# Performance work log

Measured on AMD Instinct MI355X. Metric: run time of the kernel, lower is better.

The kernel has to match this reference:

```python
import jax, jax.numpy as jnp
import numpy as np

N_NODES = 20000
N_EDGES = 160000
IN_DIM = 2048
HID = 512


def setup_inputs() -> dict:
    key = jax.random.key(0)
    ks = jax.random.split(key, 12)
    s1 = 1.0 / np.sqrt(IN_DIM)
    s2 = 1.0 / np.sqrt(HID)
    return {
        "x": jax.random.normal(ks[0], (N_NODES, IN_DIM), dtype=jnp.float32),
        "edge_index": jax.random.randint(ks[1], (2, N_EDGES), 0, N_NODES, dtype=jnp.int64),
        "W1": jax.random.uniform(ks[2], (IN_DIM, HID), jnp.float32, -s1, s1),
        "b1": jax.random.uniform(ks[3], (HID,), jnp.float32, -s1, s1),
        "W2": jax.random.uniform(ks[4], (HID, HID), jnp.float32, -s2, s2),
        "b2": jax.random.uniform(ks[5], (HID,), jnp.float32, -s2, s2),
        "Wg": jax.random.uniform(ks[6], (HID, HID), jnp.float32, -s2, s2),
        "bg": jax.random.uniform(ks[7], (HID,), jnp.float32, -s2, s2),
        "Wa": jax.random.uniform(ks[8], (HID, 1), jnp.float32, -s2, s2),
        "ba": jax.random.uniform(ks[9], (1,), jnp.float32, -s2, s2),
    }


def reference(x, edge_index, W1, b1, W2, b2, Wg, bg, Wa, ba):
    # GINConv (eps=0): h = MLP((1+eps)*x + sum_{j in N(i)} x_j)
    src, dst = edge_index[0], edge_index[1]
    agg = jax.ops.segment_sum(x[src], dst, num_segments=x.shape[0])  # [N, IN_DIM]
    h = x + agg
    h = jnp.maximum(h @ W1 + b1, 0.0) @ W2 + b2  # [N, HID]
    # Gated attention pooling scores
    A = jnp.tanh(h @ Wg + bg)                    # [N, HID]
    alpha = (A @ Wa + ba)[:, 0]                  # [N]
    att_scores = jax.nn.softmax(alpha, axis=0)   # softmax over all nodes
    return (h, att_scores)
```

## Files before the change

kernel.cpp:

```cpp
#include <hip/hip_runtime.h>

typedef __attribute__((ext_vector_type(8))) __bf16 bf16x8;
typedef __attribute__((ext_vector_type(4))) __bf16 bf16x4;
typedef __attribute__((ext_vector_type(4))) float f32x4;
typedef __attribute__((ext_vector_type(8))) unsigned short u16x8;

__device__ __forceinline__ bf16x8 cvt8(float4 a, float4 b) {
    bf16x8 o;
    o[0] = (__bf16)a.x; o[1] = (__bf16)a.y; o[2] = (__bf16)a.z; o[3] = (__bf16)a.w;
    o[4] = (__bf16)b.x; o[5] = (__bf16)b.y; o[6] = (__bf16)b.z; o[7] = (__bf16)b.w;
    return o;
}
__device__ __forceinline__ bf16x4 cvt4(f32x4 v) {
    bf16x4 o;
    o[0] = (__bf16)v[0]; o[1] = (__bf16)v[1]; o[2] = (__bf16)v[2]; o[3] = (__bf16)v[3];
    return o;
}

__device__ __forceinline__ unsigned swz(int row, int s) {
    return (unsigned)((row * 64 + s * 16) ^ ((row & 8) << 2));
}

__global__ __launch_bounds__(256) void convw_pre_kernel(const float* __restrict__ W,
                                                        char* __restrict__ out, int K) {
    int t = blockIdx.x * 256 + threadIdx.x;
    if (t >= K * 512) return;
    int k = t >> 9, n = t & 511;
    int cb = n >> 8, r = n & 255, tt = k >> 5, s = (k & 31) >> 3, e = k & 7;
    size_t off = ((size_t)cb * (K >> 5) + tt) * 16384 + swz(r, s) + e * 2;
    *(__bf16*)(out + off) = (__bf16)W[t];
}

__global__ __launch_bounds__(256) void count_kernel(const int* __restrict__ dst,
                                                    int* __restrict__ counts, int E) {
    int e = blockIdx.x * 256 + threadIdx.x;
    if (e < E) atomicAdd(&counts[dst[e]], 1);
}

__global__ __launch_bounds__(1024) void scan_kernel(const int* __restrict__ counts,
                                                    int* __restrict__ offs, int N) {
    __shared__ int wsum[16], wpre[16];
    const int CH = 20;
    int tid = threadIdx.x, lane = tid & 63, wv = tid >> 6;
    int base = tid * CH;
    int s = 0;
    for (int i = 0; i < CH; i++) { int idx = base + i; s += (idx < N) ? counts[idx] : 0; }
    int run = s;
#pragma unroll
    for (int o = 1; o < 64; o <<= 1) { int v = __shfl_up(run, o, 64); if (lane >= o) run += v; }
    if (lane == 63) wsum[wv] = run;
    __syncthreads();
    if (tid == 0) { int acc = 0; for (int w = 0; w < 16; w++) { wpre[w] = acc; acc += wsum[w]; } }
    __syncthreads();
    int pre = wpre[wv] + (run - s);
    for (int i = 0; i < CH; i++) {
        int idx = base + i;
        if (idx <= N) offs[idx] = pre;
        pre += (idx < N) ? counts[idx] : 0;
    }
}

__global__ __launch_bounds__(256) void bucket_kernel(const int* __restrict__ src,
                                                     const int* __restrict__ dst,
                                                     const int* __restrict__ offs,
                                                     int* __restrict__ cursor,
                                                     int* __restrict__ eids, int E) {
    int e = blockIdx.x * 256 + threadIdx.x;
    if (e >= E) return;
    int d = dst[e];
    int pos = atomicAdd(&cursor[d], 1);
    eids[offs[d] + pos] = src[e];
}

__global__ __launch_bounds__(256) void addy_kernel(const __bf16* __restrict__ y0,
                                                   const __bf16* __restrict__ y1,
                                                   __bf16* __restrict__ y) {
    size_t i = ((size_t)blockIdx.x * 256 + threadIdx.x) * 8;
    bf16x8 a = *(const bf16x8*)(y0 + i);
    bf16x8 b = *(const bf16x8*)(y1 + i);
    bf16x8 o;
#pragma unroll
    for (int j = 0; j < 8; j++) o[j] = (__bf16)((float)a[j] + (float)b[j]);
    *(bf16x8*)(y + i) = o;
}

__global__ __launch_bounds__(256) void gather_h1_kernel(const __bf16* __restrict__ y,
                                                        const int* __restrict__ offs,
                                                        const int* __restrict__ eids,
                                                        const float* __restrict__ b1,
                                                        __bf16* __restrict__ h1b) {
    const int node = blockIdx.x * 4 + (threadIdx.x >> 6);
    const int c = (threadIdx.x & 63) * 8;
    float s[8];
    bf16x8 v = *(const bf16x8*)(y + (size_t)node * 512 + c);
#pragma unroll
    for (int j = 0; j < 8; j++) s[j] = (float)v[j];
    const int beg = offs[node], end = offs[node + 1];
    for (int k = beg; k < end; k++) {
        int sn = eids[k];
        bf16x8 u = *(const bf16x8*)(y + (size_t)sn * 512 + c);
#pragma unroll
        for (int j = 0; j < 8; j++) s[j] += (float)u[j];
    }
    bf16x8 o;
#pragma unroll
    for (int j = 0; j < 8; j++) o[j] = (__bf16)fmaxf(s[j] + b1[c + j], 0.f);
    *(bf16x8*)(h1b + (size_t)node * 512 + c) = o;
}

__global__ __launch_bounds__(256) void gemm1_kernel(const float* __restrict__ X,
                                                    const char* __restrict__ Bpre,
                                                    __bf16* __restrict__ Ybase, int M) {
    constexpr int KDIM = 2048, NT2 = 16;
    __shared__ char smem[16384];
    const int tid = threadIdx.x, lane = tid & 63, wv = tid >> 6;
    const int fr = lane & 15, sec = lane >> 4, hi4 = (lane >> 4) * 4;
    const long row0 = (long)blockIdx.x * 64;
    const int kh = blockIdx.z;
    const char* Bp = Bpre + ((size_t)blockIdx.y * 64 + (size_t)kh * 32) * 16384;
    __bf16* Y = Ybase + (size_t)kh * 10240000;

    f32x4 acc[4][4];
#pragma unroll
    for (int m = 0; m < 4; m++)
#pragma unroll
        for (int n = 0; n < 4; n++)
#pragma unroll
            for (int r = 0; r < 4; r++) acc[m][n][r] = 0.f;

    const int ar_ = tid >> 2, ks = tid & 3;
    const unsigned awz = swz(ar_, ks);
    long arow = row0 + ar_; if (arow > (long)M - 1) arow = M - 1;
    const float* Ap = X + arow * KDIM + kh * 1024;

#define ASEC(b) (smem + (b) * 8192)
#define LOAD_A4(d0, d1, d2, d3, t) do {                      \
        const float* p_ = Ap + (t) * 64 + ks * 8;            \
        d0 = *(const float4*)(p_);                           \
        d1 = *(const float4*)(p_ + 4);                       \
        d2 = *(const float4*)(p_ + 32);                      \
        d3 = *(const float4*)(p_ + 36);                      \
    } while (0)

    {
        float4 a0, a1, a2, a3;
        LOAD_A4(a0, a1, a2, a3, 0);
        *(bf16x8*)(ASEC(0) + awz) = cvt8(a0, a1);
        *(bf16x8*)(ASEC(0) + 4096 + awz) = cvt8(a2, a3);
    }
    asm volatile("s_waitcnt lgkmcnt(0)" ::: "memory");
    __builtin_amdgcn_s_barrier();

    int cur = 0;
    for (int tt = 0; tt < NT2; tt++) {
        const bool more = (tt + 1 < NT2);
        float4 a0, a1, a2, a3;
        if (more) LOAD_A4(a0, a1, a2, a3, tt + 1);
#pragma unroll
        for (int h = 0; h < 2; h++) {
            const char* bt = Bp + (size_t)(tt * 2 + h) * 16384;
            bf16x8 wf[4], xf[4];
#pragma unroll
            for (int m = 0; m < 4; m++)
                wf[m] = *(const bf16x8*)(bt + swz(wv * 64 + m * 16 + fr, sec));
#pragma unroll
            for (int n = 0; n < 4; n++)
                xf[n] = *(const bf16x8*)(ASEC(cur) + h * 4096 + swz(n * 16 + fr, sec));
#pragma unroll
            for (int m = 0; m < 4; m++)
#pragma unroll
                for (int n = 0; n < 4; n++)
                    acc[m][n] = __builtin_amdgcn_mfma_f32_16x16x32_bf16(wf[m], xf[n], acc[m][n], 0, 0, 0);
        }
        if (more) {
            const int nxt = cur ^ 1;
            *(bf16x8*)(ASEC(nxt) + awz) = cvt8(a0, a1);
            *(bf16x8*)(ASEC(nxt) + 4096 + awz) = cvt8(a2, a3);
            asm volatile("s_waitcnt lgkmcnt(0)" ::: "memory");
            __builtin_amdgcn_s_barrier();
            cur = nxt;
        }
    }
#undef ASEC
#undef LOAD_A4

#pragma unroll
    for (int n = 0; n < 4; n++) {
        long node = row0 + n * 16 + fr;
        if (node < M) {
#pragma unroll
            for (int m = 0; m < 4; m++) {
                int col = blockIdx.y * 256 + wv * 64 + m * 16 + hi4;
                *(bf16x4*)(Y + node * 512 + col) = cvt4(acc[m][n]);
            }
        }
    }
}

__global__ __launch_bounds__(512) void mlp23_kernel(const __bf16* __restrict__ H1,
                                                    const char* __restrict__ W2p,
                                                    const float* __restrict__ b2,
                                                    const char* __restrict__ Wgp,
                                                    const float* __restrict__ bg,
                                                    const float* __restrict__ Wa,
                                                    float* __restrict__ Hout,
                                                    float* __restrict__ alpha) {
    constexpr int NT2 = 8;
    __shared__ char smem[41216];
    char* Hs = smem + 8192;
    float* aS = (float*)(smem + 40960);
    const int tid = threadIdx.x, lane = tid & 63, wv = tid >> 6;
    const int fr = lane & 15, sec = lane >> 4, hi4 = (lane >> 4) * 4;
    const long row0 = (long)blockIdx.x * 32;
    const int cbv = wv >> 2, rbase = (wv & 3) * 64;

    if (tid < 32) aS[tid] = 0.f;

    const int b16 = tid * 16;
    const int sh = b16 >> 11;
    const int bb = b16 & 2047;
    const int srow = bb >> 6;
    const int soff = bb & 63;
    const int ss = (soff ^ ((srow & 8) << 2)) >> 4;
    const __bf16* ApH = H1 + (row0 + srow) * 512 + sh * 32 + ss * 8;

#define ASEC(b) (smem + (b) * 4096)

    f32x4 acc[4][2];
#pragma unroll
    for (int m = 0; m < 4; m++)
#pragma unroll
        for (int n = 0; n < 2; n++)
#pragma unroll
            for (int r = 0; r < 4; r++) acc[m][n][r] = 0.f;

    if (tid < 256) {
        u16x8 v = *(const u16x8*)(ApH);
        *(u16x8*)(ASEC(0) + b16) = v;
    }
    asm volatile("s_waitcnt lgkmcnt(0)" ::: "memory");
    __builtin_amdgcn_s_barrier();

    int cur = 0;
    for (int tt = 0; tt < NT2; tt++) {
        u16x8 av;
        const bool more = (tt + 1 < NT2);
        if (more && tid < 256) av = *(const u16x8*)(ApH + (tt + 1) * 64);
#pragma unroll
        for (int h = 0; h < 2; h++) {
            const char* bt = W2p + ((size_t)cbv * 16 + tt * 2 + h) * 16384;
            bf16x8 wf[4], xf[2];
#pragma unroll
            for (int m = 0; m < 4; m++)
                wf[m] = *(const bf16x8*)(bt + swz(rbase + m * 16 + fr, sec));
#pragma unroll
            for (int n = 0; n < 2; n++)
                xf[n] = *(const bf16x8*)(ASEC(cur) + h * 2048 + swz(n * 16 + fr, sec));
#pragma unroll
            for (int m = 0; m < 4; m++)
#pragma unroll
                for (int n = 0; n < 2; n++)
                    acc[m][n] = __builtin_amdgcn_mfma_f32_16x16x32_bf16(wf[m], xf[n], acc[m][n], 0, 0, 0);
        }
        if (more) {
            const int nxt = cur ^ 1;
            if (tid < 256) *(u16x8*)(ASEC(nxt) + b16) = av;
            asm volatile("s_waitcnt lgkmcnt(0)" ::: "memory");
            __builtin_amdgcn_s_barrier();
            cur = nxt;
        }
    }

#pragma unroll
    for (int n = 0; n < 2; n++) {
        int node = n * 16 + fr;
        long gnode = row0 + node;
#pragma unroll
        for (int m = 0; m < 4; m++) {
            int hc = wv * 64 + m * 16 + hi4;
            f32x4 bv = *(const f32x4*)(b2 + hc);
            f32x4 v = acc[m][n] + bv;
            *(f32x4*)(Hout + gnode * 512 + hc) = v;
            int tt = hc >> 5, sk = (hc & 31) >> 3, e = hc & 7;
            *(bf16x4*)(Hs + tt * 2048 + swz(node, sk) + e * 2) = cvt4(v);
        }
    }
    asm volatile("s_waitcnt lgkmcnt(0)" ::: "memory");
    __builtin_amdgcn_s_barrier();

    f32x4 acc2[4][2];
#pragma unroll
    for (int m = 0; m < 4; m++)
#pragma unroll
        for (int n = 0; n < 2; n++)
#pragma unroll
            for (int r = 0; r < 4; r++) acc2[m][n][r] = 0.f;

    for (int g = 0; g < 16; g++) {
        const char* bt = Wgp + ((size_t)cbv * 16 + g) * 16384;
        bf16x8 wf[4], xf[2];
#pragma unroll
        for (int m = 0; m < 4; m++)
            wf[m] = *(const bf16x8*)(bt + swz(rbase + m * 16 + fr, sec));
#pragma unroll
        for (int n = 0; n < 2; n++)
            xf[n] = *(const bf16x8*)(Hs + g * 2048 + swz(n * 16 + fr, sec));
#pragma unroll
        for (int m = 0; m < 4; m++)
#pragma unroll
            for (int n = 0; n < 2; n++)
                acc2[m][n] = __builtin_amdgcn_mfma_f32_16x16x32_bf16(wf[m], xf[n], acc2[m][n], 0, 0, 0);
    }
#undef ASEC

#pragma unroll
    for (int n = 0; n < 2; n++) {
        float s = 0.f;
#pragma unroll
        for (int m = 0; m < 4; m++) {
            int gc = wv * 64 + m * 16 + hi4;
            f32x4 bgv = *(const f32x4*)(bg + gc);
            f32x4 wav = *(const f32x4*)(Wa + gc);
#pragma unroll
            for (int r = 0; r < 4; r++)
                s += tanhf(acc2[m][n][r] + bgv[r]) * wav[r];
        }
        s += __shfl_xor(s, 16, 64);
        s += __shfl_xor(s, 32, 64);
        if (sec == 0) atomicAdd(&aS[n * 16 + fr], s);
    }
    __syncthreads();
    if (tid < 32) alpha[row0 + tid] = aS[tid];
}

__global__ __launch_bounds__(1024) void softmax_kernel(const float* __restrict__ alpha,
                                                       float* __restrict__ att, int N) {
    __shared__ float red[16];
    __shared__ float bc[2];
    int tid = threadIdx.x, lane = tid & 63, wv = tid >> 6;
    float m = -3.4e38f;
    for (int i = tid; i < N; i += 1024) m = fmaxf(m, alpha[i]);
#pragma unroll
    for (int o = 32; o > 0; o >>= 1) m = fmaxf(m, __shfl_xor(m, o, 64));
    if (lane == 0) red[wv] = m;
    __syncthreads();
    if (tid == 0) {
        float mm = red[0];
        for (int i = 1; i < 16; i++) mm = fmaxf(mm, red[i]);
        bc[0] = mm;
    }
    __syncthreads();
    float Mx = bc[0];
    float s = 0.f;
    for (int i = tid; i < N; i += 1024) s += expf(alpha[i] - Mx);
#pragma unroll
    for (int o = 32; o > 0; o >>= 1) s += __shfl_xor(s, o, 64);
    if (lane == 0) red[wv] = s;
    __syncthreads();
    if (tid == 0) {
        float ss = 0.f;
        for (int i = 0; i < 16; i++) ss += red[i];
        bc[1] = ss;
    }
    __syncthreads();
    float inv = 1.f / bc[1];
    for (int i = tid; i < N; i += 1024) att[i] = expf(alpha[i] - Mx) * inv;
}

extern "C" void kernel_launch(void* const* d_in, const int* in_sizes, int n_in,
                              void* d_out, int out_size, void* d_ws, size_t ws_size,
                              hipStream_t stream) {
    const float* x  = (const float*)d_in[0];
    const int*   ei = (const int*)d_in[1];
    const float* W1 = (const float*)d_in[2];
    const float* b1 = (const float*)d_in[3];
    const float* W2 = (const float*)d_in[4];
    const float* b2 = (const float*)d_in[5];
    const float* Wg = (const float*)d_in[6];
    const float* bg = (const float*)d_in[7];
    const float* Wa = (const float*)d_in[8];

    const int M = 20000, IN = 2048, H = 512, E = 160000;

    char* ws = (char*)d_ws;
    __bf16* yp    = (__bf16*)ws;
    __bf16* ysum  = (__bf16*)(ws + 40960000);
    char*  W1p    = ws + 61440000;
    char*  W2p    = ws + 63537152;
    char*  Wgp    = ws + 64061440;
    __bf16* h1b   = (__bf16*)(ws + 64585728);
    float* alpha  = (float*)(ws + 85065728);
    int*   counts = (int*)(ws + 85145728);
    int*   offs   = (int*)(ws + 85225728);
    int*   cursor = (int*)(ws + 85305732);
    int*   eids   = (int*)(ws + 85385732);

    float* hout = (float*)d_out;
    float* att  = hout + (size_t)M * H;

    convw_pre_kernel<<<4096, 256, 0, stream>>>(W1, W1p, IN);
    convw_pre_kernel<<<1024, 256, 0, stream>>>(W2, W2p, H);
    convw_pre_kernel<<<1024, 256, 0, stream>>>(Wg, Wgp, H);

    hipMemsetAsync(counts, 0, M * 4, stream);
    count_kernel<<<(E + 255) / 256, 256, 0, stream>>>(ei + E, counts, E);
    scan_kernel<<<1, 1024, 0, stream>>>(counts, offs, M);
    hipMemsetAsync(cursor, 0, M * 4, stream);
    bucket_kernel<<<(E + 255) / 256, 256, 0, stream>>>(ei, ei + E, offs, cursor, eids, E);

    gemm1_kernel<<<dim3(313, 2, 2), 256, 0, stream>>>(x, W1p, yp, M);
    addy_kernel<<<5000, 256, 0, stream>>>(yp, yp + 10240000, ysum);

    gather_h1_kernel<<<5000, 256, 0, stream>>>(ysum, offs, eids, b1, h1b);

    mlp23_kernel<<<625, 512, 0, stream>>>(h1b, W2p, b2, Wgp, bg, Wa, hout, alpha);

    softmax_kernel<<<1, 1024, 0, stream>>>(alpha, att, M);
}
```

Baseline: 290.1 us.

## Restructure gemm1 to 4-way split-K with full A tile staged in LDS

The first GEMM now uses 512-thread blocks that load the whole 64x512 A slice, converted to bf16, into 64KB of LDS up front. The K dimension is split into four chunks instead of two, and the double-buffered A pipeline is replaced by a single barrier. Each block now covers all 512 output columns across 8 waves, so every A load is shared by both column halves and x is read from global memory only once. The cost is four bf16 partial outputs, which doubles the partial-sum traffic summed by addy4, plus a larger LDS footprint that may reduce occupancy. The global loads no longer overlap with the MFMA work.

```diff
diff --git a/kernel.cpp b/kernel.cpp
--- a/kernel.cpp
+++ b/kernel.cpp
@@ -72,15 +72,17 @@
     eids[offs[d] + pos] = src[e];
 }
 
-__global__ __launch_bounds__(256) void addy_kernel(const __bf16* __restrict__ y0,
-                                                   const __bf16* __restrict__ y1,
-                                                   __bf16* __restrict__ y) {
+__global__ __launch_bounds__(256) void addy4_kernel(const __bf16* __restrict__ p,
+                                                    __bf16* __restrict__ y) {
     size_t i = ((size_t)blockIdx.x * 256 + threadIdx.x) * 8;
-    bf16x8 a = *(const bf16x8*)(y0 + i);
-    bf16x8 b = *(const bf16x8*)(y1 + i);
+    bf16x8 a = *(const bf16x8*)(p + i);
+    bf16x8 b = *(const bf16x8*)(p + 10240000 + i);
+    bf16x8 c = *(const bf16x8*)(p + 20480000 + i);
+    bf16x8 d = *(const bf16x8*)(p + 30720000 + i);
     bf16x8 o;
 #pragma unroll
-    for (int j = 0; j < 8; j++) o[j] = (__bf16)((float)a[j] + (float)b[j]);
+    for (int j = 0; j < 8; j++)
+        o[j] = (__bf16)(((float)a[j] + (float)b[j]) + ((float)c[j] + (float)d[j]));
     *(bf16x8*)(y + i) = o;
 }
 
@@ -108,18 +110,32 @@
     *(bf16x8*)(h1b + (size_t)node * 512 + c) = o;
 }
 
-__global__ __launch_bounds__(256) void gemm1_kernel(const float* __restrict__ X,
-                                                    const char* __restrict__ Bpre,
-                                                    __bf16* __restrict__ Ybase, int M) {
-    constexpr int KDIM = 2048, NT2 = 16;
-    __shared__ char smem[16384];
+__global__ __launch_bounds__(512, 4) void gemm1_kernel(const float* __restrict__ X,
+                                                       const char* __restrict__ Bpre,
+                                                       __bf16* __restrict__ Ybase, int M) {
+    extern __shared__ char smem[];
     const int tid = threadIdx.x, lane = tid & 63, wv = tid >> 6;
     const int fr = lane & 15, sec = lane >> 4, hi4 = (lane >> 4) * 4;
     const long row0 = (long)blockIdx.x * 64;
-    const int kh = blockIdx.z;
-    const char* Bp = Bpre + ((size_t)blockIdx.y * 64 + (size_t)kh * 32) * 16384;
+    const int kh = blockIdx.y;
+    const int cb = wv >> 2, rbase = (wv & 3) * 64;
+    const char* Bp = Bpre + ((size_t)cb * 64 + (size_t)kh * 16) * 16384;
     __bf16* Y = Ybase + (size_t)kh * 10240000;
 
+#pragma unroll
+    for (int j = 0; j < 8; j++) {
+        int b = tid * 16 + j * 8192;
+        int tt = b >> 12, bb = b & 4095;
+        int row = bb >> 6, soff = bb & 63;
+        int s = (soff ^ ((row & 8) << 2)) >> 4;
+        long arow = row0 + row; if (arow > (long)M - 1) arow = M - 1;
+        const float* p = X + arow * 2048 + kh * 512 + tt * 32 + s * 8;
+        float4 a0 = *(const float4*)p;
+        float4 a1 = *(const float4*)(p + 4);
+        *(bf16x8*)(smem + b) = cvt8(a0, a1);
+    }
+    __syncthreads();
+
     f32x4 acc[4][4];
 #pragma unroll
     for (int m = 0; m < 4; m++)
@@ -128,61 +144,22 @@
 #pragma unroll
             for (int r = 0; r < 4; r++) acc[m][n][r] = 0.f;
 
-    const int ar_ = tid >> 2, ks = tid & 3;
-    const unsigned awz = swz(ar_, ks);
-    long arow = row0 + ar_; if (arow > (long)M - 1) arow = M - 1;
-    const float* Ap = X + arow * KDIM + kh * 1024;
-
-#define ASEC(b) (smem + (b) * 8192)
-#define LOAD_A4(d0, d1, d2, d3, t) do {                      \
-        const float* p_ = Ap + (t) * 64 + ks * 8;            \
-        d0 = *(const float4*)(p_);                           \
-        d1 = *(const float4*)(p_ + 4);                       \
-        d2 = *(const float4*)(p_ + 32);                      \
-        d3 = *(const float4*)(p_ + 36);                      \
-    } while (0)
-
-    {
-        float4 a0, a1, a2, a3;
-        LOAD_A4(a0, a1, a2, a3, 0);
-        *(bf16x8*)(ASEC(0) + awz) = cvt8(a0, a1);
-        *(bf16x8*)(ASEC(0) + 4096 + awz) = cvt8(a2, a3);
-    }
-    asm volatile("s_waitcnt lgkmcnt(0)" ::: "memory");
-    __builtin_amdgcn_s_barrier();
-
-    int cur = 0;
-    for (int tt = 0; tt < NT2; tt++) {
-        const bool more = (tt + 1 < NT2);
-        float4 a0, a1, a2, a3;
-        if (more) LOAD_A4(a0, a1, a2, a3, tt + 1);
-#pragma unroll
-        for (int h = 0; h < 2; h++) {
-            const char* bt = Bp + (size_t)(tt * 2 + h) * 16384;
-            bf16x8 wf[4], xf[4];
-#pragma unroll
-            for (int m = 0; m < 4; m++)
-                wf[m] = *(const bf16x8*)(bt + swz(wv * 64 + m * 16 + fr, sec));
+    for (int tt = 0; tt < 16; tt++) {
+        const char* at = smem + tt * 4096;
+        const char* bt = Bp + (size_t)tt * 16384;
+        bf16x8 wf[4], xf[4];
+#pragma unroll
+        for (int m = 0; m < 4; m++)
+            wf[m] = *(const bf16x8*)(bt + swz(rbase + m * 16 + fr, sec));
+#pragma unroll
+        for (int n = 0; n < 4; n++)
+            xf[n] = *(const bf16x8*)(at + swz(n * 16 + fr, sec));
+#pragma unroll
+        for (int m = 0; m < 4; m++)
 #pragma unroll
             for (int n = 0; n < 4; n++)
-                xf[n] = *(const bf16x8*)(ASEC(cur) + h * 4096 + swz(n * 16 + fr, sec));
-#pragma unroll
-            for (int m = 0; m < 4; m++)
-#pragma unroll
-                for (int n = 0; n < 4; n++)
-                    acc[m][n] = __builtin_amdgcn_mfma_f32_16x16x32_bf16(wf[m], xf[n], acc[m][n], 0, 0, 0);
-        }
-        if (more) {
-            const int nxt = cur ^ 1;
-            *(bf16x8*)(ASEC(nxt) + awz) = cvt8(a0, a1);
-            *(bf16x8*)(ASEC(nxt) + 4096 + awz) = cvt8(a2, a3);
-            asm volatile("s_waitcnt lgkmcnt(0)" ::: "memory");
-            __builtin_amdgcn_s_barrier();
-            cur = nxt;
-        }
-    }
-#undef ASEC
-#undef LOAD_A4
+                acc[m][n] = __builtin_amdgcn_mfma_f32_16x16x32_bf16(wf[m], xf[n], acc[m][n], 0, 0, 0);
+    }
 
 #pragma unroll
     for (int n = 0; n < 4; n++) {
@@ -190,7 +167,7 @@
         if (node < M) {
 #pragma unroll
             for (int m = 0; m < 4; m++) {
-                int col = blockIdx.y * 256 + wv * 64 + m * 16 + hi4;
+                int col = cb * 256 + rbase + m * 16 + hi4;
                 *(bf16x4*)(Y + node * 512 + col) = cvt4(acc[m][n]);
             }
         }
@@ -384,16 +361,16 @@
 
     char* ws = (char*)d_ws;
     __bf16* yp    = (__bf16*)ws;
-    __bf16* ysum  = (__bf16*)(ws + 40960000);
-    char*  W1p    = ws + 61440000;
-    char*  W2p    = ws + 63537152;
-    char*  Wgp    = ws + 64061440;
-    __bf16* h1b   = (__bf16*)(ws + 64585728);
-    float* alpha  = (float*)(ws + 85065728);
-    int*   counts = (int*)(ws + 85145728);
-    int*   offs   = (int*)(ws + 85225728);
-    int*   cursor = (int*)(ws + 85305732);
-    int*   eids   = (int*)(ws + 85385732);
+    __bf16* ysum  = (__bf16*)(ws + 81920000);
+    char*  W1p    = ws + 102400000;
+    char*  W2p    = ws + 104497152;
+    char*  Wgp    = ws + 105021440;
+    __bf16* h1b   = (__bf16*)(ws + 105545728);
+    float* alpha  = (float*)(ws + 126025728);
+    int*   counts = (int*)(ws + 126105728);
+    int*   offs   = (int*)(ws + 126185728);
+    int*   cursor = (int*)(ws + 126265732);
+    int*   eids   = (int*)(ws + 126345732);
 
     float* hout = (float*)d_out;
     float* att  = hout + (size_t)M * H;
@@ -408,8 +385,8 @@
     hipMemsetAsync(cursor, 0, M * 4, stream);
     bucket_kernel<<<(E + 255) / 256, 256, 0, stream>>>(ei, ei + E, offs, cursor, eids, E);
 
-    gemm1_kernel<<<dim3(313, 2, 2), 256, 0, stream>>>(x, W1p, yp, M);
-    addy_kernel<<<5000, 256, 0, stream>>>(yp, yp + 10240000, ysum);
+    gemm1_kernel<<<dim3(313, 4), 512, 65536, stream>>>(x, W1p, yp, M);
+    addy4_kernel<<<5000, 256, 0, stream>>>(yp, ysum);
 
     gather_h1_kernel<<<5000, 256, 0, stream>>>(ysum, offs, eids, b1, h1b);
 
```

New measurement: 288.4 us. Within noise of the previous version (-0.6%).
